# Kernel tuning notes

Hardware: AMD Instinct MI355X
Metric: run time of the kernel (lower is better)

## Reference

```python
import jax, jax.numpy as jnp
import numpy as np

HEAD_NUM = 8
HEAD_DIM = 32
EPS = 0.0  # torch.linalg.norm division has no eps; keep exact


def setup_inputs() -> dict:
    key = jax.random.key(0)
    k1, k2 = jax.random.split(key)
    batch_s = jax.random.normal(k1, (2048, HEAD_NUM * HEAD_DIM), dtype=jnp.float32)
    batch_ro = jax.random.normal(k2, (8192, HEAD_NUM * HEAD_DIM), dtype=jnp.float32)
    return {"batch_s": batch_s, "batch_ro": batch_ro}


def reference(batch_s, batch_ro):
    N, M = batch_s.shape[0], batch_ro.shape[0]
    s = batch_s.reshape(N, HEAD_NUM, HEAD_DIM)   # [N, H, D]
    ro = batch_ro.reshape(M, HEAD_NUM, HEAD_DIM)  # [M, H, D]
    # L2-normalize each head vector
    s = s / jnp.linalg.norm(s, axis=-1, keepdims=True)
    ro = ro / jnp.linalg.norm(ro, axis=-1, keepdims=True)
    # per-head cosine similarity: [N, M, H]
    dist = jnp.einsum('nhd,mhd->nmh', s, ro)
    # max-pool over heads -> [N, M]
    return jnp.max(dist, axis=-1)
```

## Files before the change

kernel.cpp:

```cpp
#include <hip/hip_runtime.h>

#define S_ROWS 2048
#define RO_ROWS 8192
#define HEADS 8
#define HDIM 32
#define ROWLEN 256
#define NB_S (S_ROWS / 16)
#define NB_RO (RO_ROWS / 16)

typedef __attribute__((ext_vector_type(8))) short bf16x8;
typedef __attribute__((ext_vector_type(4))) float f32x4;
typedef __attribute__((ext_vector_type(4))) short s16x4;

__device__ __forceinline__ short f32_to_bf16_rne(float f) {
    union { float f; unsigned u; } v; v.f = f;
    return (short)((v.u + 0x7fffu + ((v.u >> 16) & 1u)) >> 16);
}

__global__ __launch_bounds__(256) void mhd_normalize(const float* __restrict__ s,
                                                     const float* __restrict__ ro,
                                                     short* __restrict__ sF,
                                                     short* __restrict__ roF) {
    const int v   = blockIdx.x * 256 + threadIdx.x;
    const int dg  = v & 7;
    const int r16 = (v >> 3) & 15;
    const int u   = v >> 7;
    const int h   = u & 7;
    const int nb_all = u >> 3;
    const bool isS = nb_all < NB_S;
    const int nb  = isS ? nb_all : nb_all - NB_S;
    const int n   = nb * 16 + r16;

    const float* src = isS ? s : ro;
    f32x4 x = *(const f32x4*)(src + (size_t)n * ROWLEN + h * HDIM + dg * 4);
    float ss = x[0] * x[0] + x[1] * x[1] + x[2] * x[2] + x[3] * x[3];
    ss += __shfl_xor(ss, 1);
    ss += __shfl_xor(ss, 2);
    ss += __shfl_xor(ss, 4);
    const float inv = rsqrtf(ss);
    s16x4 r;
    r[0] = f32_to_bf16_rne(x[0] * inv);
    r[1] = f32_to_bf16_rne(x[1] * inv);
    r[2] = f32_to_bf16_rne(x[2] * inv);
    r[3] = f32_to_bf16_rne(x[3] * inv);

    short* dst = isS ? sF : roF;
    const int NB = isS ? NB_S : NB_RO;
    const int lane_in_frag = ((dg >> 1) << 4) + r16;
    const size_t off = ((size_t)(h * NB + nb) << 9) + lane_in_frag * 8 + (dg & 1) * 4;
    *(s16x4*)(dst + off) = r;
}

__global__ __launch_bounds__(512, 4) void mhd_dist(const short* __restrict__ sF,
                                                   const short* __restrict__ roF,
                                                   float* __restrict__ out) {
    __shared__ float elds[8][16][68];
    const int lane = threadIdx.x & 63;
    const int wave = threadIdx.x >> 6;
    const int wr = wave >> 1;
    const int wc = wave & 1;
    const int xcd = blockIdx.x & 7;
    const int q   = blockIdx.x >> 3;
    const int nbA = xcd * 16 + wr * 4;
    const int nbB = q * 8 + wc * 4;
    const size_t laneOff = (size_t)lane * 8;

    f32x4 rmax[4][4];
#pragma unroll
    for (int i = 0; i < 4; ++i)
#pragma unroll
        for (int j = 0; j < 4; ++j)
            rmax[i][j] = (f32x4){-3.0e38f, -3.0e38f, -3.0e38f, -3.0e38f};

#pragma unroll 1
    for (int h = 0; h < HEADS; ++h) {
        const short* aBase = sF  + ((size_t)(h * NB_S  + nbA) << 9) + laneOff;
        const short* bBase = roF + ((size_t)(h * NB_RO + nbB) << 9) + laneOff;
        bf16x8 a[4], b[4];
#pragma unroll
        for (int i = 0; i < 4; ++i) {
            a[i] = *(const bf16x8*)(aBase + ((size_t)i << 9));
            b[i] = *(const bf16x8*)(bBase + ((size_t)i << 9));
        }
#pragma unroll
        for (int i = 0; i < 4; ++i)
#pragma unroll
            for (int j = 0; j < 4; ++j) {
                f32x4 acc = {0.f, 0.f, 0.f, 0.f};
                acc = __builtin_amdgcn_mfma_f32_16x16x32_bf16(b[j], a[i], acc, 0, 0, 0);
#pragma unroll
                for (int q2 = 0; q2 < 4; ++q2)
                    rmax[i][j][q2] = fmaxf(rmax[i][j][q2], acc[q2]);
            }
    }

    const int l15 = lane & 15;
    const int kg = lane >> 4;
    float* outBase = out + (size_t)(xcd * 256 + wr * 64) * RO_ROWS
                         + q * 128 + wc * 64;
    const int srow = lane >> 4;
    const int scol = (lane & 15) * 4;
#pragma unroll
    for (int i = 0; i < 4; ++i) {
#pragma unroll
        for (int j = 0; j < 4; ++j)
            *(f32x4*)&elds[wave][l15][kg * 4 + j * 16] = rmax[i][j];
#pragma unroll
        for (int t = 0; t < 4; ++t) {
            const int rowL = t * 4 + srow;
            f32x4 vv = *(const f32x4*)&elds[wave][rowL][scol];
            *(f32x4*)(outBase + (size_t)(i * 16 + rowL) * RO_ROWS + scol) = vv;
        }
    }
}

extern "C" void kernel_launch(void* const* d_in, const int* in_sizes, int n_in,
                              void* d_out, int out_size, void* d_ws, size_t ws_size,
                              hipStream_t stream) {
    const float* batch_s  = (const float*)d_in[0];
    const float* batch_ro = (const float*)d_in[1];
    float* out = (float*)d_out;

    short* sF  = (short*)d_ws;
    short* roF = sF + (size_t)S_ROWS * ROWLEN;

    const int totalV4 = (S_ROWS + RO_ROWS) * ROWLEN / 4;
    mhd_normalize<<<totalV4 / 256, 256, 0, stream>>>(batch_s, batch_ro, sF, roF);

    mhd_dist<<<(S_ROWS / 256) * (RO_ROWS / 128), 512, 0, stream>>>(sF, roF, out);
}
```

Before: 95.94 us.

## Reshape block tile to 128x256 with block-wide LDS staging for full-row stores

Changes each block's output tile from 256x128 to 128x256 (2x4 wave grid) and swizzles block IDs so that consecutive blocks on the same XCD share tile rows. The epilogue now stages a 16x256 strip across four waves in shared memory, so each wave writes one contiguous 1 KB row segment per store instead of 256-byte pieces. This aims to improve write coalescing of the 64 MB fp32 output and L2 locality for the inputs. In exchange it adds block-wide __syncthreads in the epilogue, which serializes waves.

```diff
diff --git a/kernel.cpp b/kernel.cpp
--- a/kernel.cpp
+++ b/kernel.cpp
@@ -54,15 +54,17 @@
 __global__ __launch_bounds__(512, 4) void mhd_dist(const short* __restrict__ sF,
                                                    const short* __restrict__ roF,
                                                    float* __restrict__ out) {
-    __shared__ float elds[8][16][68];
+    __shared__ float lds[2][16][260];
     const int lane = threadIdx.x & 63;
     const int wave = threadIdx.x >> 6;
-    const int wr = wave >> 1;
-    const int wc = wave & 1;
-    const int xcd = blockIdx.x & 7;
-    const int q   = blockIdx.x >> 3;
-    const int nbA = xcd * 16 + wr * 4;
-    const int nbB = q * 8 + wc * 4;
+    const int wr = wave >> 2;
+    const int wc = wave & 3;
+    const int bid = blockIdx.x;
+    const int swz = (bid & 7) * 64 + (bid >> 3);
+    const int tile_r = swz >> 5;
+    const int tile_c = swz & 31;
+    const int nbA = tile_r * 8 + wr * 4;
+    const int nbB = tile_c * 16 + wc * 4;
     const size_t laneOff = (size_t)lane * 8;
 
     f32x4 rmax[4][4];
@@ -74,8 +76,8 @@
 
 #pragma unroll 1
     for (int h = 0; h < HEADS; ++h) {
-        const short* aBase = sF  + ((size_t)(h * NB_S  + nbA) << 9) + laneOff;
-        const short* bBase = roF + ((size_t)(h * NB_RO + nbB) << 9) + laneOff;
+        const short* aBase = sF  + (((size_t)(h * NB_S  + nbA)) << 9) + laneOff;
+        const short* bBase = roF + (((size_t)(h * NB_RO + nbB)) << 9) + laneOff;
         bf16x8 a[4], b[4];
 #pragma unroll
         for (int i = 0; i < 4; ++i) {
@@ -96,21 +98,22 @@
 
     const int l15 = lane & 15;
     const int kg = lane >> 4;
-    float* outBase = out + (size_t)(xcd * 256 + wr * 64) * RO_ROWS
-                         + q * 128 + wc * 64;
-    const int srow = lane >> 4;
-    const int scol = (lane & 15) * 4;
+    const int myrow4 = (wave & 3) * 4;
+    float* outRowBase = out + (size_t)(tile_r * 128 + wr * 64) * RO_ROWS
+                            + tile_c * 256;
 #pragma unroll
     for (int i = 0; i < 4; ++i) {
 #pragma unroll
         for (int j = 0; j < 4; ++j)
-            *(f32x4*)&elds[wave][l15][kg * 4 + j * 16] = rmax[i][j];
+            *(f32x4*)&lds[wr][l15][wc * 64 + kg * 4 + j * 16] = rmax[i][j];
+        __syncthreads();
 #pragma unroll
         for (int t = 0; t < 4; ++t) {
-            const int rowL = t * 4 + srow;
-            f32x4 vv = *(const f32x4*)&elds[wave][rowL][scol];
-            *(f32x4*)(outBase + (size_t)(i * 16 + rowL) * RO_ROWS + scol) = vv;
+            const int r16 = myrow4 + t;
+            f32x4 vv = *(const f32x4*)&lds[wr][r16][lane * 4];
+            *(f32x4*)(outRowBase + (size_t)(i * 16 + r16) * RO_ROWS + lane * 4) = vv;
         }
+        if (i < 3) __syncthreads();
     }
 }
 
@@ -127,5 +130,5 @@
     const int totalV4 = (S_ROWS + RO_ROWS) * ROWLEN / 4;
     mhd_normalize<<<totalV4 / 256, 256, 0, stream>>>(batch_s, batch_ro, sF, roF);
 
-    mhd_dist<<<(S_ROWS / 256) * (RO_ROWS / 128), 512, 0, stream>>>(sF, roF, out);
+    mhd_dist<<<(S_ROWS / 128) * (RO_ROWS / 256), 512, 0, stream>>>(sF, roF, out);
 }
```

Measured after the change: 101.7 us. 6.0% more time.
